# Performance work log

Hardware: AMD Instinct MI355X
Metric: run time of the kernel (lower is better)

Reference implementation:

```python
import jax, jax.numpy as jnp
import numpy as np

B, N, H = 8, 1024, 768
NH, HD = 12, 64  # num heads, head size
E = 131072       # total edges (avg degree 16)
N_REL = 30


def setup_inputs() -> dict:
    key = jax.random.key(0)
    ks = jax.random.split(key, 8)
    node_states = jax.random.normal(ks[0], (B, N, H), dtype=jnp.float32)
    eb = jax.random.randint(ks[1], (E,), 0, B, dtype=jnp.int32)
    ei = jax.random.randint(ks[2], (E,), 0, N, dtype=jnp.int32)
    ej = jax.random.randint(ks[3], (E,), 0, N, dtype=jnp.int32)
    er = jax.random.randint(ks[4], (E,), 0, N_REL, dtype=jnp.int32)
    edge_indices = jnp.stack([eb, ei, ej, er], axis=0)  # (4, E)
    scale = 1.0 / np.sqrt(H)
    Wq = jax.random.normal(ks[5], (H, H), dtype=jnp.float32) * scale
    Wk = jax.random.normal(ks[6], (H, H), dtype=jnp.float32) * scale
    Wv = jax.random.normal(ks[7], (H, H), dtype=jnp.float32) * scale
    return {"node_states": node_states, "edge_indices": edge_indices,
            "Wq": Wq, "Wk": Wk, "Wv": Wv}


def reference(node_states, edge_indices, Wq, Wk, Wv):
    # node_states: (B, N, H); edge_indices: (4, E) rows = (batch, head_node, tail_node, relation)
    b, i, j = edge_indices[0], edge_indices[1], edge_indices[2]
    q = (node_states @ Wq).reshape(B, N, NH, HD)
    k = (node_states @ Wk).reshape(B, N, NH, HD)
    v = (node_states @ Wv).reshape(B, N, NH, HD)
    qe = q[b, i]  # (E, NH, HD) gather at head nodes
    ke = k[b, j]  # (E, NH, HD) gather at tail nodes
    scores = jnp.einsum('ehd,ehd->eh', qe, ke) * (1.0 / np.sqrt(HD))  # (E, NH)
    seg = b * N + i  # segment = (batch, head_node)
    nseg = B * N
    smax = jax.ops.segment_max(scores, seg, num_segments=nseg)  # (nseg, NH)
    ex = jnp.exp(scores - smax[seg])
    denom = jax.ops.segment_sum(ex, seg, num_segments=nseg)
    probs = ex / jnp.maximum(denom[seg], 1e-9)  # (E, NH) edge softmax over tail nodes
    ve = v[b, j]  # (E, NH, HD)
    out_e = (probs[:, :, None] * ve).reshape(E, NH * HD)
    out = jax.ops.segment_sum(out_e, seg, num_segments=nseg)  # sum over tail dim
    return out.reshape(B, N, H)
```

## Files before the change

kernel.cpp:

```cpp
#include <hip/hip_runtime.h>
#include <hip/hip_fp16.h>

#define BB 8
#define NN 1024
#define HH 768
#define NHEAD 12
#define HD 64
#define NSEG 8192
#define QKVN 2304
#define MAXDEG 64

typedef unsigned short u16;
typedef __attribute__((ext_vector_type(8))) _Float16 f16x8;
typedef __attribute__((ext_vector_type(4))) float f32x4;
typedef __attribute__((ext_vector_type(4))) unsigned int u32x4;
typedef __attribute__((ext_vector_type(2))) unsigned int u32x2;

__device__ __forceinline__ u16 f2h(float f) {
  _Float16 h = (_Float16)f;
  return __builtin_bit_cast(u16, h);
}
__device__ __forceinline__ __half2 h2(unsigned int w) {
  return __builtin_bit_cast(__half2, w);
}

#define CAST_BLKS (NSEG * HH / 4 / 256)
#define TW_BLKS   ((QKVN / 32) * (HH / 32))
#define BUILD_BLKS 512

__global__ void prep_kernel(const float* __restrict__ X, u16* __restrict__ Xb,
                            const float* __restrict__ Wq, const float* __restrict__ Wk,
                            const float* __restrict__ Wv, u16* __restrict__ Wt,
                            const int* __restrict__ EI, int* __restrict__ cursor,
                            int* __restrict__ tailrow, int E) {
  const int bid = blockIdx.x;
  if (bid < CAST_BLKS) {
    int i = bid * 256 + threadIdx.x;
    float4 f = ((const float4*)X)[i];
    ushort4 o;
    o.x = f2h(f.x); o.y = f2h(f.y); o.z = f2h(f.z); o.w = f2h(f.w);
    ((ushort4*)Xb)[i] = o;
  } else if (bid < CAST_BLKS + TW_BLKS) {
    __shared__ float tile[32][33];
    int t = bid - CAST_BLKS;
    int n0 = (t % (QKVN / 32)) * 32;
    int k0 = (t / (QKVN / 32)) * 32;
    const float* W = (n0 < HH) ? Wq : (n0 < 2 * HH ? Wk : Wv);
    int nb = n0 - (n0 < HH ? 0 : (n0 < 2 * HH ? HH : 2 * HH));
    int tx = threadIdx.x & 31, ty = threadIdx.x >> 5;
#pragma unroll
    for (int r = 0; r < 4; ++r)
      tile[ty + 8 * r][tx] = W[(k0 + ty + 8 * r) * HH + nb + tx];
    __syncthreads();
#pragma unroll
    for (int r = 0; r < 4; ++r)
      Wt[(n0 + ty + 8 * r) * HH + k0 + tx] = f2h(tile[tx][ty + 8 * r]);
  } else {
    int e = (bid - CAST_BLKS - TW_BLKS) * 256 + threadIdx.x;
    if (e >= E) return;
    int b = EI[e];
    int seg = b * NN + EI[E + e];
    int j = EI[2 * E + e];
    int pos = atomicAdd(&cursor[seg], 1);
    if (pos < MAXDEG) tailrow[seg * MAXDEG + pos] = b * NN + j;
  }
}

#define BM 128
#define BN 128
#define BK 32
#define NITER (HH / BK)

__global__ __launch_bounds__(256) void gemm_kernel(const u16* __restrict__ Xb,
                                                   const u16* __restrict__ Wt,
                                                   u16* __restrict__ QKV) {
  __shared__ u16 As[3][BM * BK];
  __shared__ u16 Bs[3][BN * BK];
  const int tid = threadIdx.x;
  const int wave = tid >> 6;
  const int lane = tid & 63;
  const int bid = blockIdx.x;
  const int mt = (bid & 7) * 8 + ((bid >> 3) & 7);
  const int nt = bid >> 6;
  const int m0 = mt * BM;
  const int n0 = nt * BN;
  const int wr = wave >> 1;
  const int wc = wave & 1;
  const int quad = lane >> 4;
  const int l15 = lane & 15;

  f32x4 acc[4][4] = {};

  const int srow = wave * 16 + (lane >> 2);
  const int scol = (((lane & 3) ^ ((lane >> 3) & 3)) << 3);
  const int rswz = quad ^ ((l15 >> 1) & 3);

  auto stage = [&](int buf, int kt) {
#pragma unroll
    for (int p = 0; p < 2; ++p) {
      const u16* ga = Xb + (m0 + p * 64 + srow) * HH + kt + scol;
      const u16* gb = Wt + (n0 + p * 64 + srow) * HH + kt + scol;
      u16* la = As[buf] + p * 2048 + wave * 512;
      u16* lb = Bs[buf] + p * 2048 + wave * 512;
      __builtin_amdgcn_global_load_lds(
          (const __attribute__((address_space(1))) unsigned int*)(unsigned long long)ga,
          (__attribute__((address_space(3))) unsigned int*)(unsigned long long)la, 16, 0, 0);
      __builtin_amdgcn_global_load_lds(
          (const __attribute__((address_space(1))) unsigned int*)(unsigned long long)gb,
          (__attribute__((address_space(3))) unsigned int*)(unsigned long long)lb, 16, 0, 0);
    }
  };

  stage(0, 0);
  stage(1, BK);

#pragma unroll 3
  for (int it = 0; it < NITER; ++it) {
    if (it != NITER - 1) {
      asm volatile("s_waitcnt vmcnt(4)" ::: "memory");
    } else {
      asm volatile("s_waitcnt vmcnt(0)" ::: "memory");
    }
    asm volatile("s_barrier" ::: "memory");
    if (it + 2 < NITER) stage((it + 2) % 3, (it + 2) * BK);

    const int b = it % 3;
    f16x8 afr[4], bfr[4];
#pragma unroll
    for (int mi = 0; mi < 4; ++mi) {
      int m = wr * 64 + mi * 16 + l15;
      afr[mi] = *(const f16x8*)(As[b] + m * BK + rswz * 8);
    }
#pragma unroll
    for (int ni = 0; ni < 4; ++ni) {
      int n = wc * 64 + ni * 16 + l15;
      bfr[ni] = *(const f16x8*)(Bs[b] + n * BK + rswz * 8);
    }
#pragma unroll
    for (int mi = 0; mi < 4; ++mi)
#pragma unroll
      for (int ni = 0; ni < 4; ++ni)
        acc[mi][ni] = __builtin_amdgcn_mfma_f32_16x16x32_f16(afr[mi], bfr[ni], acc[mi][ni], 0, 0, 0);
  }

#pragma unroll
  for (int mi = 0; mi < 4; ++mi)
#pragma unroll
    for (int ni = 0; ni < 4; ++ni) {
      int col = n0 + wc * 64 + ni * 16 + l15;
#pragma unroll
      for (int r = 0; r < 4; ++r) {
        int row = m0 + wr * 64 + mi * 16 + quad * 4 + r;
        QKV[row * QKVN + col] = f2h(acc[mi][ni][r]);
      }
    }
}

__global__ __launch_bounds__(256) void attn_kernel(const u16* __restrict__ QKV,
                                                   const int* __restrict__ tailrow,
                                                   const int* __restrict__ cursor,
                                                   float* __restrict__ out) {
  __shared__ float sm[2 * 16 * 64];
  const int wv = threadIdx.x >> 6;
  const int lane = threadIdx.x & 63;
  const int sIb = wv >> 1;
  const int half = wv & 1;
  const int blk = (blockIdx.x & 7) * (NSEG / 16) + (blockIdx.x >> 3);
  const int seg = blk * 2 + sIb;
  const int base = seg * MAXDEG;
  int cnt = cursor[seg];
  if (cnt > MAXDEG) cnt = MAXDEG;
  const int myn = (cnt > half) ? ((cnt - half + 1) >> 1) : 0;

  int myidx = (lane < cnt) ? tailrow[base + lane] : 0;

  const u16* qrow = QKV + seg * QKVN;
  __half2 q1[4], q2[2];
  {
    u32x4 qa = *(const u32x4*)(qrow + lane * 8);
    u32x2 qb = *(const u32x2*)(qrow + 512 + lane * 4);
    const __half2 sc = __float2half2_rn(0.125f);
#pragma unroll
    for (int i = 0; i < 4; ++i) q1[i] = __hmul2(h2(qa[i]), sc);
    q2[0] = __hmul2(h2(qb[0]), sc);
    q2[1] = __hmul2(h2(qb[1]), sc);
  }

  float m1 = -__builtin_inff(), l1 = 0.f;
  float m2 = -__builtin_inff(), l2 = 0.f;
  __half2 o1[4] = {}, o2[2] = {};

  auto loadkv = [&](int row, u32x4& k1, u32x2& k2, u32x4& v1, u32x2& v2) {
    const u16* kp = QKV + row * QKVN + HH;
    k1 = *(const u32x4*)(kp + lane * 8);
    k2 = *(const u32x2*)(kp + 512 + lane * 4);
    v1 = *(const u32x4*)(kp + HH + lane * 8);
    v2 = *(const u32x2*)(kp + HH + 512 + lane * 4);
  };

  auto process = [&](u32x4 k1, u32x2 k2, u32x4 v1, u32x2 v2) {
    __half2 a1 = __hmul2(q1[0], h2(k1[0]));
    a1 = __hfma2(q1[1], h2(k1[1]), a1);
    a1 = __hfma2(q1[2], h2(k1[2]), a1);
    a1 = __hfma2(q1[3], h2(k1[3]), a1);
    float s1 = __low2float(a1) + __high2float(a1);
    s1 += __shfl_xor(s1, 1, 64);
    s1 += __shfl_xor(s1, 2, 64);
    s1 += __shfl_xor(s1, 4, 64);
    __half2 a2 = __hmul2(q2[0], h2(k2[0]));
    a2 = __hfma2(q2[1], h2(k2[1]), a2);
    float s2 = __low2float(a2) + __high2float(a2);
    s2 += __shfl_xor(s2, 1, 64);
    s2 += __shfl_xor(s2, 2, 64);
    s2 += __shfl_xor(s2, 4, 64);
    s2 += __shfl_xor(s2, 8, 64);
    {
      float mn = fmaxf(m1, s1);
      float al = __expf(m1 - mn);
      float ex = __expf(s1 - mn);
      l1 = l1 * al + ex;
      __half2 ah = __float2half2_rn(al), eh = __float2half2_rn(ex);
#pragma unroll
      for (int i = 0; i < 4; ++i)
        o1[i] = __hfma2(o1[i], ah, __hmul2(h2(v1[i]), eh));
      m1 = mn;
    }
    {
      float mn = fmaxf(m2, s2);
      float al = __expf(m2 - mn);
      float ex = __expf(s2 - mn);
      l2 = l2 * al + ex;
      __half2 ah = __float2half2_rn(al), eh = __float2half2_rn(ex);
      o2[0] = __hfma2(o2[0], ah, __hmul2(h2(v2[0]), eh));
      o2[1] = __hfma2(o2[1], ah, __hmul2(h2(v2[1]), eh));
      m2 = mn;
    }
  };

  if (myn > 0) {
    u32x4 k1c, v1c, k1n, v1n, k1n2, v1n2;
    u32x2 k2c, v2c, k2n, v2n, k2n2, v2n2;
    loadkv(__shfl(myidx, half, 64), k1c, k2c, v1c, v2c);
    if (myn > 1) loadkv(__shfl(myidx, half + 2, 64), k1n, k2n, v1n, v2n);
    for (int t = 0; t < myn; ++t) {
      if (t + 2 < myn)
        loadkv(__shfl(myidx, half + 2 * (t + 2), 64), k1n2, k2n2, v1n2, v2n2);
      process(k1c, k2c, v1c, v2c);
      k1c = k1n; k2c = k2n; v1c = v1n; v2c = v2n;
      k1n = k1n2; k2n = k2n2; v1n = v1n2; v2n = v2n2;
    }
  }

  float of1[8], of2[4];
#pragma unroll
  for (int i = 0; i < 4; ++i) {
    of1[2 * i] = __low2float(o1[i]);
    of1[2 * i + 1] = __high2float(o1[i]);
  }
#pragma unroll
  for (int i = 0; i < 2; ++i) {
    of2[2 * i] = __low2float(o2[i]);
    of2[2 * i + 1] = __high2float(o2[i]);
  }

  float* sb = sm + sIb * 16 * 64;
  if (half == 1) {
    sb[0 * 64 + lane] = m1;  sb[1 * 64 + lane] = l1;
    sb[2 * 64 + lane] = m2;  sb[3 * 64 + lane] = l2;
#pragma unroll
    for (int i = 0; i < 8; ++i) sb[(4 + i) * 64 + lane] = of1[i];
#pragma unroll
    for (int i = 0; i < 4; ++i) sb[(12 + i) * 64 + lane] = of2[i];
  }
  __syncthreads();
  if (half == 0) {
    float mB1 = sb[0 * 64 + lane], lB1 = sb[1 * 64 + lane];
    float mB2 = sb[2 * 64 + lane], lB2 = sb[3 * 64 + lane];

    float res1[8], res2[4];
    {
      float mn = fmaxf(fmaxf(m1, mB1), -1e30f);
      float aA = __expf(m1 - mn), aB = __expf(mB1 - mn);
      float l = l1 * aA + lB1 * aB;
      float inv = 1.f / fmaxf(l, 1e-9f);
#pragma unroll
      for (int i = 0; i < 8; ++i)
        res1[i] = (of1[i] * aA + sb[(4 + i) * 64 + lane] * aB) * inv;
    }
    {
      float mn = fmaxf(fmaxf(m2, mB2), -1e30f);
      float aA = __expf(m2 - mn), aB = __expf(mB2 - mn);
      float l = l2 * aA + lB2 * aB;
      float inv = 1.f / fmaxf(l, 1e-9f);
#pragma unroll
      for (int i = 0; i < 4; ++i)
        res2[i] = (of2[i] * aA + sb[(12 + i) * 64 + lane] * aB) * inv;
    }

    float* op = out + seg * HH;
    float4 r0 = {res1[0], res1[1], res1[2], res1[3]};
    float4 r1 = {res1[4], res1[5], res1[6], res1[7]};
    float4 r2 = {res2[0], res2[1], res2[2], res2[3]};
    ((float4*)(op + lane * 8))[0] = r0;
    ((float4*)(op + lane * 8))[1] = r1;
    *(float4*)(op + 512 + lane * 4) = r2;
  }
}

extern "C" void kernel_launch(void* const* d_in, const int* in_sizes, int n_in,
                              void* d_out, int out_size, void* d_ws, size_t ws_size,
                              hipStream_t stream) {
  const float* X  = (const float*)d_in[0];
  const int*   EI = (const int*)d_in[1];
  const float* Wq = (const float*)d_in[2];
  const float* Wk = (const float*)d_in[3];
  const float* Wv = (const float*)d_in[4];
  float* out = (float*)d_out;
  const int E = in_sizes[1] / 4;

  char* ws = (char*)d_ws;
  int* cursor  = (int*)(ws);
  int* tailrow = (int*)(ws + 32768);
  u16* Xb      = (u16*)(ws + 2129920);
  u16* Wt      = (u16*)(ws + 14712832);
  u16* QKV     = (u16*)(ws + 18251776);

  hipMemsetAsync(cursor, 0, NSEG * 4, stream);
  prep_kernel<<<CAST_BLKS + TW_BLKS + BUILD_BLKS, 256, 0, stream>>>(
      X, Xb, Wq, Wk, Wv, Wt, EI, cursor, tailrow, E);
  gemm_kernel<<<(QKVN / BN) * (NSEG / BM), 256, 0, stream>>>(Xb, Wt, QKV);
  attn_kernel<<<NSEG / 2, 256, 0, stream>>>(QKV, tailrow, cursor, out);
}
```

Baseline: 167.2 us.

## Split each segment's edges across four waves instead of two

The attention kernel now assigns one segment per 256-thread block, and all four waves process interleaved edges of that segment, where before two waves shared each segment. The per-wave online-softmax partial states are merged by wave 0 through a larger shared-memory buffer. The goal is a shorter serial edge loop per wave, giving more memory-level parallelism for the gather-bound K/V loads. The cost is twice as many blocks, more shared memory, a longer merge step, and more idle waves when a segment has a small degree (average about 16).

```diff
diff --git a/kernel.cpp b/kernel.cpp
--- a/kernel.cpp
+++ b/kernel.cpp
@@ -160,17 +160,14 @@
                                                    const int* __restrict__ tailrow,
                                                    const int* __restrict__ cursor,
                                                    float* __restrict__ out) {
-  __shared__ float sm[2 * 16 * 64];
+  __shared__ float sm[3 * 16 * 64];
   const int wv = threadIdx.x >> 6;
   const int lane = threadIdx.x & 63;
-  const int sIb = wv >> 1;
-  const int half = wv & 1;
-  const int blk = (blockIdx.x & 7) * (NSEG / 16) + (blockIdx.x >> 3);
-  const int seg = blk * 2 + sIb;
+  const int seg = (blockIdx.x & 7) * (NSEG / 8) + (blockIdx.x >> 3);
   const int base = seg * MAXDEG;
   int cnt = cursor[seg];
   if (cnt > MAXDEG) cnt = MAXDEG;
-  const int myn = (cnt > half) ? ((cnt - half + 1) >> 1) : 0;
+  const int myn = (cnt > wv) ? ((cnt - wv + 3) >> 2) : 0;
 
   int myidx = (lane < cnt) ? tailrow[base + lane] : 0;
 
@@ -240,11 +237,11 @@
   if (myn > 0) {
     u32x4 k1c, v1c, k1n, v1n, k1n2, v1n2;
     u32x2 k2c, v2c, k2n, v2n, k2n2, v2n2;
-    loadkv(__shfl(myidx, half, 64), k1c, k2c, v1c, v2c);
-    if (myn > 1) loadkv(__shfl(myidx, half + 2, 64), k1n, k2n, v1n, v2n);
+    loadkv(__shfl(myidx, wv, 64), k1c, k2c, v1c, v2c);
+    if (myn > 1) loadkv(__shfl(myidx, wv + 4, 64), k1n, k2n, v1n, v2n);
     for (int t = 0; t < myn; ++t) {
       if (t + 2 < myn)
-        loadkv(__shfl(myidx, half + 2 * (t + 2), 64), k1n2, k2n2, v1n2, v2n2);
+        loadkv(__shfl(myidx, wv + 4 * (t + 2), 64), k1n2, k2n2, v1n2, v2n2);
       process(k1c, k2c, v1c, v2c);
       k1c = k1n; k2c = k2n; v1c = v1n; v2c = v2n;
       k1n = k1n2; k2n = k2n2; v1n = v1n2; v2n = v2n2;
@@ -263,8 +260,8 @@
     of2[2 * i + 1] = __high2float(o2[i]);
   }
 
-  float* sb = sm + sIb * 16 * 64;
-  if (half == 1) {
+  if (wv > 0) {
+    float* sb = sm + (wv - 1) * 1024;
     sb[0 * 64 + lane] = m1;  sb[1 * 64 + lane] = l1;
     sb[2 * 64 + lane] = m2;  sb[3 * 64 + lane] = l2;
 #pragma unroll
@@ -273,28 +270,47 @@
     for (int i = 0; i < 4; ++i) sb[(12 + i) * 64 + lane] = of2[i];
   }
   __syncthreads();
-  if (half == 0) {
-    float mB1 = sb[0 * 64 + lane], lB1 = sb[1 * 64 + lane];
-    float mB2 = sb[2 * 64 + lane], lB2 = sb[3 * 64 + lane];
-
+  if (wv == 0) {
+    float mn1 = fmaxf(m1, -1e30f), mn2 = fmaxf(m2, -1e30f);
+#pragma unroll
+    for (int j = 0; j < 3; ++j) {
+      mn1 = fmaxf(mn1, sm[j * 1024 + 0 * 64 + lane]);
+      mn2 = fmaxf(mn2, sm[j * 1024 + 2 * 64 + lane]);
+    }
     float res1[8], res2[4];
     {
-      float mn = fmaxf(fmaxf(m1, mB1), -1e30f);
-      float aA = __expf(m1 - mn), aB = __expf(mB1 - mn);
-      float l = l1 * aA + lB1 * aB;
+      float a0 = __expf(m1 - mn1);
+      float l = l1 * a0;
+#pragma unroll
+      for (int i = 0; i < 8; ++i) res1[i] = of1[i] * a0;
+#pragma unroll
+      for (int j = 0; j < 3; ++j) {
+        const float* sb = sm + j * 1024;
+        float aj = __expf(sb[0 * 64 + lane] - mn1);
+        l += sb[1 * 64 + lane] * aj;
+#pragma unroll
+        for (int i = 0; i < 8; ++i) res1[i] += sb[(4 + i) * 64 + lane] * aj;
+      }
       float inv = 1.f / fmaxf(l, 1e-9f);
 #pragma unroll
-      for (int i = 0; i < 8; ++i)
-        res1[i] = (of1[i] * aA + sb[(4 + i) * 64 + lane] * aB) * inv;
+      for (int i = 0; i < 8; ++i) res1[i] *= inv;
     }
     {
-      float mn = fmaxf(fmaxf(m2, mB2), -1e30f);
-      float aA = __expf(m2 - mn), aB = __expf(mB2 - mn);
-      float l = l2 * aA + lB2 * aB;
+      float a0 = __expf(m2 - mn2);
+      float l = l2 * a0;
+#pragma unroll
+      for (int i = 0; i < 4; ++i) res2[i] = of2[i] * a0;
+#pragma unroll
+      for (int j = 0; j < 3; ++j) {
+        const float* sb = sm + j * 1024;
+        float aj = __expf(sb[2 * 64 + lane] - mn2);
+        l += sb[3 * 64 + lane] * aj;
+#pragma unroll
+        for (int i = 0; i < 4; ++i) res2[i] += sb[(12 + i) * 64 + lane] * aj;
+      }
       float inv = 1.f / fmaxf(l, 1e-9f);
 #pragma unroll
-      for (int i = 0; i < 4; ++i)
-        res2[i] = (of2[i] * aA + sb[(12 + i) * 64 + lane] * aB) * inv;
+      for (int i = 0; i < 4; ++i) res2[i] *= inv;
     }
 
     float* op = out + seg * HH;
@@ -329,5 +345,5 @@
   prep_kernel<<<CAST_BLKS + TW_BLKS + BUILD_BLKS, 256, 0, stream>>>(
       X, Xb, Wq, Wk, Wv, Wt, EI, cursor, tailrow, E);
   gemm_kernel<<<(QKVN / BN) * (NSEG / BM), 256, 0, stream>>>(Xb, Wt, QKV);
-  attn_kernel<<<NSEG / 2, 256, 0, stream>>>(QKV, tailrow, cursor, out);
-}
+  attn_kernel<<<NSEG, 256, 0, stream>>>(QKV, tailrow, cursor, out);
+}
```

After: 166.0 us. Within noise of the previous version (-0.7%).
